# Kernel optimization log

Measured on AMD Instinct MI355X. Metric: run time of the kernel, lower is better.

The kernel has to match this reference:

```python
import jax, jax.numpy as jnp
import numpy as np

ALPHA = 0.15  # top-k fraction (forward default)


def setup_inputs() -> dict:
    key = jax.random.key(0)
    k1, k2, k3 = jax.random.split(key, 3)
    B, N, D = 8, 1024, 256
    x = jax.random.normal(k1, (B, N, D), dtype=jnp.float32)
    # torch nn.Linear(dim, H*head_dim, bias=False); stored here as [D, H*head_dim]
    W_src = jax.random.normal(k2, (D, D), dtype=jnp.float32) * (1.0 / np.sqrt(D))
    W_tgt = jax.random.normal(k3, (D, D), dtype=jnp.float32) * (1.0 / np.sqrt(D))
    return {"x": x, "W_src": W_src, "W_tgt": W_tgt}


def _topk_mask(adj, k):
    # adj: [B,H,N,N]; exact scatter of 1.0 at top-k indices along last axis
    B, H, N, _ = adj.shape
    _, idx = jax.lax.top_k(adj, k)              # [B,H,N,k]
    bi = jnp.arange(B)[:, None, None, None]
    hi = jnp.arange(H)[None, :, None, None]
    ni = jnp.arange(N)[None, None, :, None]
    mask = jnp.zeros_like(adj).at[bi, hi, ni, idx].set(1.0)
    return mask


def reference(x, W_src, W_tgt):
    # directed=True path of DirectedGraphLearner.forward
    B, N, D = x.shape
    H, head_dim = 4, D // 4
    k = max(1, int(ALPHA * N))
    src = (x @ W_src).reshape(B, N, H, head_dim)
    tgt = (x @ W_tgt).reshape(B, N, H, head_dim)
    adj = jnp.einsum('bihd,bjhd->bhij', src, tgt)
    adj = jax.nn.gelu(adj, approximate=False)    # torch F.gelu default = exact erf
    mask = _topk_mask(adj, k)
    return adj * mask
```

## Files before the change

kernel.cpp:

```cpp
#include <hip/hip_runtime.h>
#include <math.h>


#define KSEL 153u
#define EPSK 61000u

typedef __attribute__((ext_vector_type(8))) short short8v;
typedef __attribute__((ext_vector_type(4))) float float4v;

__device__ __forceinline__ float gelu_f32(float x) {
    return 0.5f * x * (1.0f + erff(x * 0.70710678118654752f));
}

__device__ __forceinline__ unsigned long long d2key(double v) {
    unsigned long long u = (unsigned long long)__double_as_longlong(v);
    return (u >> 63) ? ~u : (u | 0x8000000000000000ull);
}

__device__ __forceinline__ unsigned lkeyf(float v) {
    float q = fmaf(v, 33554432.0f, 2147483648.0f);
    q = fminf(fmaxf(q, 0.0f), 4294967040.0f);
    return (unsigned)q;
}

__device__ __forceinline__ unsigned short b16(float x) {
    unsigned u = __float_as_uint(x);
    u += 0x7FFFu + ((u >> 16) & 1u);
    return (unsigned short)(u >> 16);
}
__device__ __forceinline__ float bf2f(unsigned short h) {
    return __uint_as_float(((unsigned)h) << 16);
}
__device__ __forceinline__ unsigned pk2(float a, float b) {
    return (unsigned)b16(a) | ((unsigned)b16(b) << 16);
}

#define LGKM0()                                             \
    do {                                                    \
        asm volatile("s_waitcnt lgkmcnt(0)" ::: "memory");  \
        __builtin_amdgcn_sched_barrier(0);                  \
    } while (0)

template <bool W32>
__global__ __launch_bounds__(256) void k1_proj(const float* __restrict__ x,
                                               const float* __restrict__ Wsrc,
                                               const float* __restrict__ Wtgt,
                                               double* __restrict__ ws,
                                               unsigned short* __restrict__ th,
                                               unsigned short* __restrict__ tl) {
    __shared__ float xs[32 * 68];
    __shared__ float wsh[32 * 68];
    const int t = threadIdx.x;
    const int bx = blockIdx.x;
    const int by = blockIdx.y;
    const int col0 = (by & 3) * 64;
    const float* __restrict__ W = (by < 4) ? Wsrc : Wtgt;
    double* __restrict__ outp = ws + ((by < 4) ? 0 : 2097152);

    double acc[4][4];
#pragma unroll
    for (int i = 0; i < 4; ++i)
#pragma unroll
        for (int j = 0; j < 4; ++j) acc[i][j] = 0.0;

    const int m_loc = (t & 15) * 4;
    const int c_loc = (t >> 4) * 4;

    for (int kt = 0; kt < 8; ++kt) {
        __syncthreads();
#pragma unroll
        for (int it = 0; it < 2; ++it) {
            int f4 = t + 256 * it;
            int m = f4 >> 3, k4 = f4 & 7;
            float4 v = *reinterpret_cast<const float4*>(&x[(bx * 64 + m) * 256 + kt * 32 + 4 * k4]);
            xs[(4 * k4 + 0) * 68 + m] = v.x;
            xs[(4 * k4 + 1) * 68 + m] = v.y;
            xs[(4 * k4 + 2) * 68 + m] = v.z;
            xs[(4 * k4 + 3) * 68 + m] = v.w;
        }
#pragma unroll
        for (int it = 0; it < 2; ++it) {
            int f4 = t + 256 * it;
            int k = f4 >> 4, c4 = f4 & 15;
            *reinterpret_cast<float4*>(&wsh[k * 68 + 4 * c4]) =
                *reinterpret_cast<const float4*>(&W[(kt * 32 + k) * 256 + col0 + 4 * c4]);
        }
        __syncthreads();
#pragma unroll
        for (int kk = 0; kk < 32; ++kk) {
            float4 a = *reinterpret_cast<const float4*>(&xs[kk * 68 + m_loc]);
            float4 b = *reinterpret_cast<const float4*>(&wsh[kk * 68 + c_loc]);
            double ad[4] = {a.x, a.y, a.z, a.w};
            double bd[4] = {b.x, b.y, b.z, b.w};
#pragma unroll
            for (int i = 0; i < 4; ++i)
#pragma unroll
                for (int j = 0; j < 4; ++j) acc[i][j] += ad[i] * bd[j];
        }
    }
    const int hd = by & 3;
#pragma unroll
    for (int i = 0; i < 4; ++i) {
        int m = bx * 64 + m_loc + i;
        int b = m >> 10, n = m & 1023;
        int bhd = b * 4 + hd;
        size_t base = ((size_t)(bhd * 1024 + n)) * 64 + c_loc;
        double2 v01, v23;
        v01.x = acc[i][0]; v01.y = acc[i][1];
        v23.x = acc[i][2]; v23.y = acc[i][3];
        *reinterpret_cast<double2*>(&outp[base]) = v01;
        *reinterpret_cast<double2*>(&outp[base + 2]) = v23;
        if (W32 && by >= 4) {
            float f0 = (float)acc[i][0], f1 = (float)acc[i][1];
            float f2 = (float)acc[i][2], f3 = (float)acc[i][3];
            unsigned short h0 = b16(f0), h1 = b16(f1), h2 = b16(f2), h3 = b16(f3);
            uint2 H, L;
            H.x = (unsigned)h0 | ((unsigned)h1 << 16);
            H.y = (unsigned)h2 | ((unsigned)h3 << 16);
            L.x = pk2(f0 - bf2f(h0), f1 - bf2f(h1));
            L.y = pk2(f2 - bf2f(h2), f3 - bf2f(h3));
            int T = n >> 4, colLow = n & 15;
            int ks = c_loc >> 5, kg = (c_loc >> 3) & 3, elem = c_loc & 7;
            size_t fidx = ((size_t)bhd * 65536) +
                          (size_t)(((T * 2 + ks) * 64 + kg * 16 + colLow) * 8 + elem);
            *reinterpret_cast<uint2*>(&th[fidx]) = H;
            *reinterpret_cast<uint2*>(&tl[fidx]) = L;
        }
    }
}

template <bool FAST>
__global__ __launch_bounds__(256, 4) void k2_fused(const double* __restrict__ srcT,
                                                   const double* __restrict__ tgtT,
                                                   const unsigned short* __restrict__ th,
                                                   const unsigned short* __restrict__ tlo,
                                                   float* __restrict__ out) {
    __shared__ __align__(16) float tr[16 * 512];

    unsigned short* sHI = reinterpret_cast<unsigned short*>(tr);
    unsigned short* sLO = sHI + 1024;

    const int t = threadIdx.x;
    const int lane = t & 63;
    const int wv = t >> 6;
    const int bid = (blockIdx.x & 7) * 256 + (blockIdx.x >> 3);
    const int bh = bid >> 6;
    const int itile = bid & 63;
    const int row0 = itile * 16;
    const int r0 = 4 * wv;
    const size_t tgtBase = (size_t)bh * 65536;
    const unsigned short* __restrict__ thb = th + tgtBase;
    const unsigned short* __restrict__ tlb = tlo + tgtBase;

    {
        int r = t >> 4, dq = (t & 15) * 4;
        const double* sp = &srcT[((size_t)bh * 1024 + row0 + r) * 64 + dq];
        double2 a = *reinterpret_cast<const double2*>(sp);
        double2 b = *reinterpret_cast<const double2*>(sp + 2);
        float f0 = (float)a.x, f1 = (float)a.y, f2 = (float)b.x, f3 = (float)b.y;
        unsigned short h0 = b16(f0), h1 = b16(f1), h2 = b16(f2), h3 = b16(f3);
        int s = dq >> 3;
        int idx = r * 64 + ((s ^ (r & 7)) << 3) + (dq & 7);
        uint2 H, L;
        H.x = (unsigned)h0 | ((unsigned)h1 << 16);
        H.y = (unsigned)h2 | ((unsigned)h3 << 16);
        L.x = pk2(f0 - bf2f(h0), f1 - bf2f(h1));
        L.y = pk2(f2 - bf2f(h2), f3 - bf2f(h3));
        *reinterpret_cast<uint2*>(&sHI[idx]) = H;
        *reinterpret_cast<uint2*>(&sLO[idx]) = L;
    }
    __syncthreads();

    short8v Ah[2], Al[2];
#pragma unroll
    for (int ks = 0; ks < 2; ++ks) {
        int idxA = (lane & 15) * 64 + (((4 * ks + (lane >> 4)) ^ (lane & 7)) << 3);
        Ah[ks] = *reinterpret_cast<const short8v*>(&sHI[idxA]);
        Al[ks] = *reinterpret_cast<const short8v*>(&sLO[idxA]);
    }

    const int colA = lane & 15;
    const int kgrp = lane >> 4;
    float vals[4][16];

#pragma unroll
    for (int h = 0; h < 2; ++h) {
        float4v acc[8];
#pragma unroll
        for (int a = 0; a < 8; ++a) acc[a] = (float4v){0.f, 0.f, 0.f, 0.f};

#pragma unroll
        for (int u = 0; u < 8; ++u) {
            const int T = 32 * h + 4 * u + wv;
#pragma unroll
            for (int ks = 0; ks < 2; ++ks) {
                short8v Bh, Bl;
                if (FAST) {
                    const size_t fbase = (size_t)(((T * 2 + ks) * 64 + lane) * 8);
                    Bh = *reinterpret_cast<const short8v*>(&thb[fbase]);
                    Bl = *reinterpret_cast<const short8v*>(&tlb[fbase]);
                } else {
                    const size_t cbase = (size_t)(16 * T + colA) * 64 + kgrp * 8;
                    const double* gp = &tgtT[tgtBase + cbase + 32 * ks];
                    double2 d0 = *reinterpret_cast<const double2*>(gp);
                    double2 d1 = *reinterpret_cast<const double2*>(gp + 2);
                    double2 d2 = *reinterpret_cast<const double2*>(gp + 4);
                    double2 d3 = *reinterpret_cast<const double2*>(gp + 6);
                    float f[8] = {(float)d0.x, (float)d0.y, (float)d1.x, (float)d1.y,
                                  (float)d2.x, (float)d2.y, (float)d3.x, (float)d3.y};
                    unsigned short hh[8];
#pragma unroll
                    for (int e = 0; e < 8; ++e) hh[e] = b16(f[e]);
                    unsigned Hw[4], Lw[4];
#pragma unroll
                    for (int e = 0; e < 4; ++e) {
                        Hw[e] = (unsigned)hh[2 * e] | ((unsigned)hh[2 * e + 1] << 16);
                        Lw[e] = pk2(f[2 * e] - bf2f(hh[2 * e]), f[2 * e + 1] - bf2f(hh[2 * e + 1]));
                    }
                    Bh = *reinterpret_cast<const short8v*>(Hw);
                    Bl = *reinterpret_cast<const short8v*>(Lw);
                }
                acc[u] = __builtin_amdgcn_mfma_f32_16x16x32_bf16(Ah[ks], Bh, acc[u], 0, 0, 0);
                acc[u] = __builtin_amdgcn_mfma_f32_16x16x32_bf16(Al[ks], Bh, acc[u], 0, 0, 0);
                acc[u] = __builtin_amdgcn_mfma_f32_16x16x32_bf16(Ah[ks], Bl, acc[u], 0, 0, 0);
            }
        }

        __syncthreads();
#pragma unroll
        for (int u = 0; u < 8; ++u) {
            int colh = 16 * (4 * u + wv) + colA;
#pragma unroll
            for (int reg = 0; reg < 4; ++reg) {
                int row = 4 * kgrp + reg;
                tr[row * 512 + (colh ^ ((kgrp & 1) << 4))] = acc[u][reg];
            }
        }
        __syncthreads();
        const int rsw = (wv & 1) << 4;
#pragma unroll
        for (int ri = 0; ri < 4; ++ri) {
            int row = r0 + ri;
#pragma unroll
            for (int mm = 0; mm < 8; ++mm) {
                int colh = lane + 64 * mm;
                vals[ri][8 * h + mm] = tr[row * 512 + (colh ^ rsw)];
            }
        }
    }

    __syncthreads();

    unsigned* histw = reinterpret_cast<unsigned*>(tr) + 256 * wv;
    unsigned* cjp = histw + 128;
    unsigned long long* ckp = reinterpret_cast<unsigned long long*>(histw);
    unsigned* ccp = histw + 192;
    const size_t outBase = ((size_t)bh * 1024 + row0 + r0) * 1024;

#pragma unroll
    for (int ri = 0; ri < 4; ++ri) {
        unsigned ul[16];
#pragma unroll
        for (int m = 0; m < 16; ++m) ul[m] = lkeyf(vals[ri][m]);

        unsigned prefA = 0u, maskA = 0u, rk = KSEL;
#pragma unroll 1
        for (int p = 1; p >= 0; --p) {
            const int sh = 16 + 8 * p;
            *reinterpret_cast<uint4*>(&histw[4 * lane]) = make_uint4(0u, 0u, 0u, 0u);
            LGKM0();
#pragma unroll
            for (int m = 0; m < 16; ++m) {
                if ((ul[m] & maskA) == prefA)
                    atomicAdd(&histw[(ul[m] >> sh) & 255u], 1u);
            }
            LGKM0();
            unsigned h0 = histw[4 * lane + 0], h1 = histw[4 * lane + 1];
            unsigned h2 = histw[4 * lane + 2], h3 = histw[4 * lane + 3];
            unsigned S = h0 + h1 + h2 + h3;
            unsigned inc = S;
#pragma unroll
            for (int off = 1; off < 64; off <<= 1) {
                unsigned o = __shfl_down(inc, off, 64);
                inc = (lane + off < 64) ? (inc + o) : inc;
            }
            unsigned above = inc - S;
            bool found = (above < rk) && (rk <= inc);
            unsigned long long bal = __ballot(found);
            int L = __ffsll(bal) - 1;
            unsigned hh[4];
            hh[0] = __shfl(h0, L, 64);
            hh[1] = __shfl(h1, L, 64);
            hh[2] = __shfl(h2, L, 64);
            hh[3] = __shfl(h3, L, 64);
            unsigned cum = __shfl(above, L, 64);
            int bsel = -1;
#pragma unroll
            for (int q = 3; q >= 0; --q) {
                if (bsel < 0) {
                    if (rk <= cum + hh[q]) {
                        bsel = q;
                        rk = rk - cum;
                    } else {
                        cum += hh[q];
                    }
                }
            }
            prefA |= (unsigned)(4 * L + bsel) << sh;
            maskA |= 0xFFu << sh;
        }

        const unsigned klo = prefA - EPSK;
        const unsigned khi = prefA + 65535u + EPSK;

        int ch = 0, cb = 0;
#pragma unroll
        for (int m = 0; m < 16; ++m) {
            ch += (ul[m] > khi) ? 1 : 0;
            cb += (ul[m] >= klo && ul[m] <= khi) ? 1 : 0;
        }
#pragma unroll
        for (int off = 32; off; off >>= 1) {
            ch += __shfl_xor(ch, off, 64);
            cb += __shfl_xor(cb, off, 64);
        }
        const unsigned need = KSEL - (unsigned)ch;
        const bool fastp = ((unsigned)cb == need);

        unsigned long long selMask = 0ull;
        unsigned cidx[16];
        if (!fastp) {
            if (lane == 0) *ccp = 0u;
            LGKM0();
#pragma unroll
            for (int m = 0; m < 16; ++m) {
                cidx[m] = 0xFFFFFFFFu;
                if (ul[m] >= klo && ul[m] <= khi) {
                    unsigned idx = atomicAdd(ccp, 1u);
                    cidx[m] = idx;
                    if (idx < 64u) cjp[idx] = (unsigned)(lane + 64 * m);
                }
            }
            LGKM0();
            unsigned g = *ccp;
            if (g > 64u) g = 64u;
            unsigned rnk = need;
            if (lane < (int)g) {
                unsigned j = cjp[lane];
                const double2* sp = reinterpret_cast<const double2*>(
                    &srcT[((size_t)bh * 1024 + row0 + r0 + ri) * 64]);
                const double2* tp = reinterpret_cast<const double2*>(&tgtT[tgtBase + (size_t)j * 64]);
                double a2 = 0.0;
#pragma unroll 8
                for (int d2 = 0; d2 < 32; ++d2) {
                    double2 aa = sp[d2], bb = tp[d2];
                    a2 = fma(aa.x, bb.x, fma(aa.y, bb.y, a2));
                }
                ckp[lane] = d2key(a2);
            }
            LGKM0();
            if (lane < (int)g) {
                unsigned long long myk = ckp[lane];
                unsigned myj = cjp[lane];
                rnk = 0;
                for (unsigned i = 0; i < g; ++i) {
                    unsigned long long ki = ckp[i];
                    rnk += (ki > myk || (ki == myk && cjp[i] < myj)) ? 1u : 0u;
                }
            }
            selMask = __ballot(lane < (int)g && rnk < need);
        }

        const size_t rowBase = outBase + (size_t)ri * 1024;
#pragma unroll
        for (int m = 0; m < 16; ++m) {
            bool sel;
            if (ul[m] > khi) sel = true;
            else if (ul[m] < klo) sel = false;
            else sel = fastp ? true
                             : ((cidx[m] < 64u) ? (((selMask >> cidx[m]) & 1ull) != 0ull) : false);
            float v = vals[ri][m];
            float g = 0.0f;
            if (sel) g = (v > 3.0f) ? v : gelu_f32(v);
            out[rowBase + (unsigned)(lane + 64 * m)] = g;
        }
    }
}

extern "C" void kernel_launch(void* const* d_in, const int* in_sizes, int n_in,
                              void* d_out, int out_size, void* d_ws, size_t ws_size,
                              hipStream_t stream) {
    const float* x = (const float*)d_in[0];
    const float* Wsrc = (const float*)d_in[1];
    const float* Wtgt = (const float*)d_in[2];
    float* out = (float*)d_out;
    double* ws = (double*)d_ws;
    unsigned short* th = (unsigned short*)((char*)d_ws + 33554432);
    unsigned short* tl = (unsigned short*)((char*)d_ws + 37748736);

    const bool fast = (ws_size >= 40u * 1024u * 1024u);
    dim3 g1(128, 8);
    if (fast) {
        k1_proj<true><<<g1, 256, 0, stream>>>(x, Wsrc, Wtgt, ws, th, tl);
        k2_fused<true><<<2048, 256, 0, stream>>>(ws, ws + 2097152, th, tl, out);
    } else {
        k1_proj<false><<<g1, 256, 0, stream>>>(x, Wsrc, Wtgt, ws, th, tl);
        k2_fused<false><<<2048, 256, 0, stream>>>(ws, ws + 2097152, th, tl, out);
    }
}
```

Baseline: 171.2 us.

## Split fused GEMM+top-k kernel into separate GEMM and per-row select kernels

Unfuses the score GEMM from the top-k selection. The first kernel writes raw scores to the output buffer. A new kernel then reads each row back, runs the radix select and the fp64 tie-break, and writes the masked GELU. This is meant to cut register pressure in the fused kernel and raise occupancy or parallelism for selection. In exchange it adds a full extra read and write of the 128 MB output plus an extra launch.

```diff
diff --git a/kernel.cpp b/kernel.cpp
--- a/kernel.cpp
+++ b/kernel.cpp
@@ -130,7 +130,7 @@
 }
 
 template <bool FAST>
-__global__ __launch_bounds__(256, 4) void k2_fused(const double* __restrict__ srcT,
+__global__ __launch_bounds__(256, 4) void k2a_gemm(const double* __restrict__ srcT,
                                                    const double* __restrict__ tgtT,
                                                    const unsigned short* __restrict__ th,
                                                    const unsigned short* __restrict__ tlo,
@@ -181,7 +181,7 @@
 
     const int colA = lane & 15;
     const int kgrp = lane >> 4;
-    float vals[4][16];
+    const size_t outBase = ((size_t)bh * 1024 + row0 + r0) * 1024;
 
 #pragma unroll
     for (int h = 0; h < 2; ++h) {
@@ -244,146 +244,158 @@
 #pragma unroll
             for (int mm = 0; mm < 8; ++mm) {
                 int colh = lane + 64 * mm;
-                vals[ri][8 * h + mm] = tr[row * 512 + (colh ^ rsw)];
-            }
-        }
-    }
-
-    __syncthreads();
-
-    unsigned* histw = reinterpret_cast<unsigned*>(tr) + 256 * wv;
+                out[outBase + (size_t)ri * 1024 + 512 * h + colh] =
+                    tr[row * 512 + (colh ^ rsw)];
+            }
+        }
+    }
+}
+
+__global__ __launch_bounds__(256, 4) void k2b_select(const double* __restrict__ srcT,
+                                                     const double* __restrict__ tgtT,
+                                                     float* __restrict__ out) {
+    __shared__ __align__(16) unsigned hist[4][256];
+
+    const int t = threadIdx.x;
+    const int lane = t & 63;
+    const int wv = t >> 6;
+    const int R = blockIdx.x * 4 + wv;
+    const int bh = R >> 10;
+    const size_t tgtBase = (size_t)bh * 65536;
+    const size_t base = (size_t)R * 1024;
+
+    float vals[16];
+#pragma unroll
+    for (int m = 0; m < 16; ++m) vals[m] = out[base + lane + 64 * m];
+
+    unsigned* histw = hist[wv];
     unsigned* cjp = histw + 128;
     unsigned long long* ckp = reinterpret_cast<unsigned long long*>(histw);
     unsigned* ccp = histw + 192;
-    const size_t outBase = ((size_t)bh * 1024 + row0 + r0) * 1024;
-
-#pragma unroll
-    for (int ri = 0; ri < 4; ++ri) {
-        unsigned ul[16];
-#pragma unroll
-        for (int m = 0; m < 16; ++m) ul[m] = lkeyf(vals[ri][m]);
-
-        unsigned prefA = 0u, maskA = 0u, rk = KSEL;
+
+    unsigned ul[16];
+#pragma unroll
+    for (int m = 0; m < 16; ++m) ul[m] = lkeyf(vals[m]);
+
+    unsigned prefA = 0u, maskA = 0u, rk = KSEL;
 #pragma unroll 1
-        for (int p = 1; p >= 0; --p) {
-            const int sh = 16 + 8 * p;
-            *reinterpret_cast<uint4*>(&histw[4 * lane]) = make_uint4(0u, 0u, 0u, 0u);
-            LGKM0();
-#pragma unroll
-            for (int m = 0; m < 16; ++m) {
-                if ((ul[m] & maskA) == prefA)
-                    atomicAdd(&histw[(ul[m] >> sh) & 255u], 1u);
-            }
-            LGKM0();
-            unsigned h0 = histw[4 * lane + 0], h1 = histw[4 * lane + 1];
-            unsigned h2 = histw[4 * lane + 2], h3 = histw[4 * lane + 3];
-            unsigned S = h0 + h1 + h2 + h3;
-            unsigned inc = S;
-#pragma unroll
-            for (int off = 1; off < 64; off <<= 1) {
-                unsigned o = __shfl_down(inc, off, 64);
-                inc = (lane + off < 64) ? (inc + o) : inc;
-            }
-            unsigned above = inc - S;
-            bool found = (above < rk) && (rk <= inc);
-            unsigned long long bal = __ballot(found);
-            int L = __ffsll(bal) - 1;
-            unsigned hh[4];
-            hh[0] = __shfl(h0, L, 64);
-            hh[1] = __shfl(h1, L, 64);
-            hh[2] = __shfl(h2, L, 64);
-            hh[3] = __shfl(h3, L, 64);
-            unsigned cum = __shfl(above, L, 64);
-            int bsel = -1;
-#pragma unroll
-            for (int q = 3; q >= 0; --q) {
-                if (bsel < 0) {
-                    if (rk <= cum + hh[q]) {
-                        bsel = q;
-                        rk = rk - cum;
-                    } else {
-                        cum += hh[q];
-                    }
+    for (int p = 1; p >= 0; --p) {
+        const int sh = 16 + 8 * p;
+        *reinterpret_cast<uint4*>(&histw[4 * lane]) = make_uint4(0u, 0u, 0u, 0u);
+        LGKM0();
+#pragma unroll
+        for (int m = 0; m < 16; ++m) {
+            if ((ul[m] & maskA) == prefA)
+                atomicAdd(&histw[(ul[m] >> sh) & 255u], 1u);
+        }
+        LGKM0();
+        unsigned h0 = histw[4 * lane + 0], h1 = histw[4 * lane + 1];
+        unsigned h2 = histw[4 * lane + 2], h3 = histw[4 * lane + 3];
+        unsigned S = h0 + h1 + h2 + h3;
+        unsigned inc = S;
+#pragma unroll
+        for (int off = 1; off < 64; off <<= 1) {
+            unsigned o = __shfl_down(inc, off, 64);
+            inc = (lane + off < 64) ? (inc + o) : inc;
+        }
+        unsigned above = inc - S;
+        bool found = (above < rk) && (rk <= inc);
+        unsigned long long bal = __ballot(found);
+        int L = __ffsll(bal) - 1;
+        unsigned hh[4];
+        hh[0] = __shfl(h0, L, 64);
+        hh[1] = __shfl(h1, L, 64);
+        hh[2] = __shfl(h2, L, 64);
+        hh[3] = __shfl(h3, L, 64);
+        unsigned cum = __shfl(above, L, 64);
+        int bsel = -1;
+#pragma unroll
+        for (int q = 3; q >= 0; --q) {
+            if (bsel < 0) {
+                if (rk <= cum + hh[q]) {
+                    bsel = q;
+                    rk = rk - cum;
+                } else {
+                    cum += hh[q];
                 }
             }
-            prefA |= (unsigned)(4 * L + bsel) << sh;
-            maskA |= 0xFFu << sh;
-        }
-
-        const unsigned klo = prefA - EPSK;
-        const unsigned khi = prefA + 65535u + EPSK;
-
-        int ch = 0, cb = 0;
+        }
+        prefA |= (unsigned)(4 * L + bsel) << sh;
+        maskA |= 0xFFu << sh;
+    }
+
+    const unsigned klo = prefA - EPSK;
+    const unsigned khi = prefA + 65535u + EPSK;
+
+    int ch = 0, cb = 0;
+#pragma unroll
+    for (int m = 0; m < 16; ++m) {
+        ch += (ul[m] > khi) ? 1 : 0;
+        cb += (ul[m] >= klo && ul[m] <= khi) ? 1 : 0;
+    }
+#pragma unroll
+    for (int off = 32; off; off >>= 1) {
+        ch += __shfl_xor(ch, off, 64);
+        cb += __shfl_xor(cb, off, 64);
+    }
+    const unsigned need = KSEL - (unsigned)ch;
+    const bool fastp = ((unsigned)cb == need);
+
+    unsigned long long selMask = 0ull;
+    unsigned cidx[16];
+    if (!fastp) {
+        if (lane == 0) *ccp = 0u;
+        LGKM0();
 #pragma unroll
         for (int m = 0; m < 16; ++m) {
-            ch += (ul[m] > khi) ? 1 : 0;
-            cb += (ul[m] >= klo && ul[m] <= khi) ? 1 : 0;
-        }
-#pragma unroll
-        for (int off = 32; off; off >>= 1) {
-            ch += __shfl_xor(ch, off, 64);
-            cb += __shfl_xor(cb, off, 64);
-        }
-        const unsigned need = KSEL - (unsigned)ch;
-        const bool fastp = ((unsigned)cb == need);
-
-        unsigned long long selMask = 0ull;
-        unsigned cidx[16];
-        if (!fastp) {
-            if (lane == 0) *ccp = 0u;
-            LGKM0();
-#pragma unroll
-            for (int m = 0; m < 16; ++m) {
-                cidx[m] = 0xFFFFFFFFu;
-                if (ul[m] >= klo && ul[m] <= khi) {
-                    unsigned idx = atomicAdd(ccp, 1u);
-                    cidx[m] = idx;
-                    if (idx < 64u) cjp[idx] = (unsigned)(lane + 64 * m);
-                }
-            }
-            LGKM0();
-            unsigned g = *ccp;
-            if (g > 64u) g = 64u;
-            unsigned rnk = need;
-            if (lane < (int)g) {
-                unsigned j = cjp[lane];
-                const double2* sp = reinterpret_cast<const double2*>(
-                    &srcT[((size_t)bh * 1024 + row0 + r0 + ri) * 64]);
-                const double2* tp = reinterpret_cast<const double2*>(&tgtT[tgtBase + (size_t)j * 64]);
-                double a2 = 0.0;
+            cidx[m] = 0xFFFFFFFFu;
+            if (ul[m] >= klo && ul[m] <= khi) {
+                unsigned idx = atomicAdd(ccp, 1u);
+                cidx[m] = idx;
+                if (idx < 64u) cjp[idx] = (unsigned)(lane + 64 * m);
+            }
+        }
+        LGKM0();
+        unsigned g = *ccp;
+        if (g > 64u) g = 64u;
+        unsigned rnk = need;
+        if (lane < (int)g) {
+            unsigned j = cjp[lane];
+            const double2* sp = reinterpret_cast<const double2*>(&srcT[(size_t)R * 64]);
+            const double2* tp = reinterpret_cast<const double2*>(&tgtT[tgtBase + (size_t)j * 64]);
+            double a2 = 0.0;
 #pragma unroll 8
-                for (int d2 = 0; d2 < 32; ++d2) {
-                    double2 aa = sp[d2], bb = tp[d2];
-                    a2 = fma(aa.x, bb.x, fma(aa.y, bb.y, a2));
-                }
-                ckp[lane] = d2key(a2);
-            }
-            LGKM0();
-            if (lane < (int)g) {
-                unsigned long long myk = ckp[lane];
-                unsigned myj = cjp[lane];
-                rnk = 0;
-                for (unsigned i = 0; i < g; ++i) {
-                    unsigned long long ki = ckp[i];
-                    rnk += (ki > myk || (ki == myk && cjp[i] < myj)) ? 1u : 0u;
-                }
-            }
-            selMask = __ballot(lane < (int)g && rnk < need);
-        }
-
-        const size_t rowBase = outBase + (size_t)ri * 1024;
-#pragma unroll
-        for (int m = 0; m < 16; ++m) {
-            bool sel;
-            if (ul[m] > khi) sel = true;
-            else if (ul[m] < klo) sel = false;
-            else sel = fastp ? true
-                             : ((cidx[m] < 64u) ? (((selMask >> cidx[m]) & 1ull) != 0ull) : false);
-            float v = vals[ri][m];
-            float g = 0.0f;
-            if (sel) g = (v > 3.0f) ? v : gelu_f32(v);
-            out[rowBase + (unsigned)(lane + 64 * m)] = g;
-        }
+            for (int d2 = 0; d2 < 32; ++d2) {
+                double2 aa = sp[d2], bb = tp[d2];
+                a2 = fma(aa.x, bb.x, fma(aa.y, bb.y, a2));
+            }
+            ckp[lane] = d2key(a2);
+        }
+        LGKM0();
+        unsigned rnk2 = need;
+        if (lane < (int)g) {
+            unsigned long long myk = ckp[lane];
+            unsigned myj = cjp[lane];
+            rnk2 = 0;
+            for (unsigned i = 0; i < g; ++i) {
+                unsigned long long ki = ckp[i];
+                rnk2 += (ki > myk || (ki == myk && cjp[i] < myj)) ? 1u : 0u;
+            }
+        }
+        selMask = __ballot(lane < (int)g && rnk2 < need);
+    }
+
+#pragma unroll
+    for (int m = 0; m < 16; ++m) {
+        bool sel;
+        if (ul[m] > khi) sel = true;
+        else if (ul[m] < klo) sel = false;
+        else sel = fastp ? true
+                         : ((cidx[m] < 64u) ? (((selMask >> cidx[m]) & 1ull) != 0ull) : false);
+        float v = vals[m];
+        float g = 0.0f;
+        if (sel) g = (v > 3.0f) ? v : gelu_f32(v);
+        out[base + (unsigned)(lane + 64 * m)] = g;
     }
 }
 
@@ -402,9 +414,10 @@
     dim3 g1(128, 8);
     if (fast) {
         k1_proj<true><<<g1, 256, 0, stream>>>(x, Wsrc, Wtgt, ws, th, tl);
-        k2_fused<true><<<2048, 256, 0, stream>>>(ws, ws + 2097152, th, tl, out);
+        k2a_gemm<true><<<2048, 256, 0, stream>>>(ws, ws + 2097152, th, tl, out);
     } else {
         k1_proj<false><<<g1, 256, 0, stream>>>(x, Wsrc, Wtgt, ws, th, tl);
-        k2_fused<false><<<2048, 256, 0, stream>>>(ws, ws + 2097152, th, tl, out);
-    }
-}
+        k2a_gemm<false><<<2048, 256, 0, stream>>>(ws, ws + 2097152, th, tl, out);
+    }
+    k2b_select<<<8192, 256, 0, stream>>>(ws, ws + 2097152, out);
+}
```

Result: faster. 159.2 us (-7.0%).
